# Kernel tuning notes

Hardware: AMD Instinct MI355X
Metric: run time of the kernel (lower is better)

Reference implementation:

```python
import jax, jax.numpy as jnp
import numpy as np

NEG_INF = -1e9
LN_EPS = 1e-5

N, F_IN, F_OUT, H = 4096, 128, 64, 4


def setup_inputs() -> dict:
    key = jax.random.key(0)
    ks = jax.random.split(key, 8)
    return {
        "nodes_features": jax.random.normal(ks[0], (N, F_IN), jnp.float32),
        "degree_matrix": jax.random.normal(ks[1], (N, N), jnp.float32),
        "edges_features_distance": jax.random.normal(ks[2], (N, N), jnp.float32),
        "edges_features_bond": jax.random.normal(ks[3], (N, N), jnp.float32),
        "proj_param": jax.random.normal(ks[4], (H, F_IN, F_OUT), jnp.float32) * 0.1,
        "score_src": jax.random.normal(ks[5], (H, F_OUT, 1), jnp.float32) * 0.1,
        "score_tgt": jax.random.normal(ks[6], (H, F_OUT, 1), jnp.float32) * 0.1,
        "skip_w": jax.random.normal(ks[7], (H * F_OUT, F_IN), jnp.float32) * 0.1,
        "cutoff": 0,
    }


def reference(nodes_features, degree_matrix, edges_features_distance,
              edges_features_bond, proj_param, score_src, score_tgt,
              skip_w, cutoff):
    # connectivity mask: nested where on degree/bond matrices  [N, N]
    wdm = degree_matrix + edges_features_bond
    mask = jnp.where(wdm > 0, wdm,
                     jnp.where(edges_features_bond > cutoff,
                               edges_features_bond + wdm, NEG_INF))

    # per-head projection: [H, N, F_out]
    proj = jnp.einsum('nf,hfo->hno', nodes_features, proj_param)

    # scalar scores per node per head: [H, N, 1]
    s_src = jnp.einsum('hno,hop->hnp', proj, score_src)
    s_tgt = jnp.einsum('hno,hop->hnp', proj, score_tgt)

    # broadcast score matrix [H, N, N]; softmax over dim=1 (as in the original)
    scores = jax.nn.leaky_relu(s_src + jnp.swapaxes(s_tgt, 1, 2), negative_slope=0.2)
    attn = jax.nn.softmax(scores + mask[None, :, :], axis=1)

    # weighted aggregation: [H, N, F_out] -> [N, H, F_out]
    out = jnp.einsum('hij,hjf->hif', attn, proj)
    out = jnp.swapaxes(out, 0, 1)

    # skip connection (F_in != F_out -> linear skip projection)
    skip = (nodes_features @ skip_w.T).reshape(-1, H, F_OUT)
    out = out + skip

    # concat heads, ELU activation (no bias: ctor passes bias=None)
    out = jax.nn.elu(out.reshape(-1, H * F_OUT))

    # fresh LayerNorm (weight=1, bias=0) over last dim of mask
    mu = jnp.mean(mask, axis=-1, keepdims=True)
    var = jnp.var(mask, axis=-1, keepdims=True)
    mask_ln = (mask - mu) / jnp.sqrt(var + LN_EPS)

    return out, mask_ln
```

## Files before the change

kernel.cpp:

```cpp
#include <hip/hip_runtime.h>
#include <math.h>

constexpr int kN  = 4096;
constexpr int kFI = 128;
constexpr int kFO = 64;
constexpr int kH  = 4;
constexpr int kHF = 256;
constexpr float kNegInf = -1e9f;
constexpr float kLnEps  = 1e-5f;
constexpr float kL2E    = 1.44269504f;

typedef short bf16x8 __attribute__((ext_vector_type(8)));
typedef float f32x4  __attribute__((ext_vector_type(4)));

__device__ __forceinline__ float lrelu(float x){ return x >= 0.f ? x : 0.2f*x; }

__device__ __forceinline__ float wave_sum(float v){
  #pragma unroll
  for (int s = 32; s > 0; s >>= 1) v += __shfl_xor(v, s, 64);
  return v;
}

__device__ __forceinline__ unsigned short f2bf(float x){
  unsigned u = __float_as_uint(x);
  u = (u + 0x7fffu + ((u >> 16) & 1u)) >> 16;
  return (unsigned short)u;
}
__device__ __forceinline__ unsigned f2bf_pk(float a, float b){
  return (unsigned)f2bf(a) | ((unsigned)f2bf(b) << 16);
}

__global__ __launch_bounds__(256) void k_tr(
    const float* __restrict__ skw, float* __restrict__ skwT)
{
  const int k  = blockIdx.x;
  const int hf = threadIdx.x;
  skwT[k*kHF + hf] = skw[hf*kFI + k];
}

__global__ __launch_bounds__(256) void k_proj(
    const float* __restrict__ nodes, const float* __restrict__ pp,
    const float* __restrict__ ssrc,  const float* __restrict__ stgt,
    const float* __restrict__ skwT,
    float* __restrict__ proj, float* __restrict__ ga, float* __restrict__ gb,
    float* __restrict__ skipo)
{
  __shared__ float feat[8][kFI];
  const int tid = threadIdx.x;
  const int n0  = blockIdx.x * 8;
  for (int idx = tid; idx < 8*kFI; idx += 256)
    feat[idx >> 7][idx & 127] = nodes[n0*kFI + idx];
  __syncthreads();
  const int h = tid >> 6, o = tid & 63;
  float accP[8], accS[8];
  #pragma unroll
  for (int n = 0; n < 8; ++n){ accP[n] = 0.f; accS[n] = 0.f; }
  for (int k0 = 0; k0 < kFI; k0 += 4){
    float p[4], w[4];
    #pragma unroll
    for (int u = 0; u < 4; ++u){
      p[u] = pp[(h*kFI + k0+u)*kFO + o];
      w[u] = skwT[(k0+u)*kHF + tid];
    }
    #pragma unroll
    for (int n = 0; n < 8; ++n){
      const float4 f4 = *(const float4*)&feat[n][k0];
      accP[n] = fmaf(f4.x, p[0], fmaf(f4.y, p[1],
                fmaf(f4.z, p[2], fmaf(f4.w, p[3], accP[n]))));
      accS[n] = fmaf(f4.x, w[0], fmaf(f4.y, w[1],
                fmaf(f4.z, w[2], fmaf(f4.w, w[3], accS[n]))));
    }
  }
  const float sa = ssrc[h*kFO + o];
  const float sb = stgt[h*kFO + o];
  #pragma unroll
  for (int n = 0; n < 8; ++n){
    proj[(h*kN + n0+n)*kFO + o] = accP[n];
    skipo[(n0+n)*kHF + tid]     = accS[n];
    const float va = wave_sum(accP[n] * sa);
    const float vb = wave_sum(accP[n] * sb);
    if (o == 0){ ga[h*kN + n0+n] = va; gb[h*kN + n0+n] = vb; }
  }
}

template<int RS>
__global__ __launch_bounds__(256) void k_colsum(
    const float* __restrict__ degm, const float* __restrict__ bondm,
    const float* __restrict__ ga,   const float* __restrict__ gb,
    const int* __restrict__ cutp,
    float* __restrict__ Spart, float* __restrict__ statg,
    float* __restrict__ maskws, int write_mask)
{
  const int j0 = (blockIdx.x * 256 + threadIdx.x) * 4;
  const int lane = threadIdx.x & 63;
  const float cut = (float)cutp[0];
  float4 bv[kH]; f32x4 sv[kH];
  #pragma unroll
  for (int h = 0; h < kH; ++h){
    bv[h] = *(const float4*)&gb[h*kN + j0];
    sv[h] = (f32x4){0.f, 0.f, 0.f, 0.f};
  }
  float msum[RS], msq[RS];
  #pragma unroll
  for (int r = 0; r < RS; ++r){ msum[r] = 0.f; msq[r] = 0.f; }

  const int i0 = blockIdx.y * RS;
  #pragma unroll
  for (int ib = 0; ib < RS; ib += 8){
    float4 dg[8], bd[8];
    #pragma unroll
    for (int u = 0; u < 8; ++u){
      const size_t off = (size_t)(i0+ib+u)*kN + j0;
      dg[u] = *(const float4*)&degm[off];
      bd[u] = *(const float4*)&bondm[off];
    }
    #pragma unroll
    for (int u = 0; u < 8; ++u){
      const int i = i0 + ib + u;
      float4 m;
      {
        float w0 = dg[u].x + bd[u].x, w1 = dg[u].y + bd[u].y;
        float w2 = dg[u].z + bd[u].z, w3 = dg[u].w + bd[u].w;
        m.x = w0 > 0.f ? w0 : (bd[u].x > cut ? bd[u].x + w0 : kNegInf);
        m.y = w1 > 0.f ? w1 : (bd[u].y > cut ? bd[u].y + w1 : kNegInf);
        m.z = w2 > 0.f ? w2 : (bd[u].z > cut ? bd[u].z + w2 : kNegInf);
        m.w = w3 > 0.f ? w3 : (bd[u].w > cut ? bd[u].w + w3 : kNegInf);
      }
      if (write_mask) *(float4*)&maskws[(size_t)i*kN + j0] = m;
      msum[ib+u] += (m.x + m.y) + (m.z + m.w);
      msq[ib+u]  += fmaf(m.x, m.x, fmaf(m.y, m.y, fmaf(m.z, m.z, m.w*m.w)));
      const float4 ml = {m.x*kL2E, m.y*kL2E, m.z*kL2E, m.w*kL2E};
      #pragma unroll
      for (int h = 0; h < kH; ++h){
        const float a = ga[h*kN + i];
        float t0 = a + bv[h].x, t1 = a + bv[h].y;
        float t2 = a + bv[h].z, t3 = a + bv[h].w;
        t0 = fmaxf(t0, 0.2f*t0); t1 = fmaxf(t1, 0.2f*t1);
        t2 = fmaxf(t2, 0.2f*t2); t3 = fmaxf(t3, 0.2f*t3);
        sv[h][0] += exp2f(fmaf(t0, kL2E, ml.x));
        sv[h][1] += exp2f(fmaf(t1, kL2E, ml.y));
        sv[h][2] += exp2f(fmaf(t2, kL2E, ml.z));
        sv[h][3] += exp2f(fmaf(t3, kL2E, ml.w));
      }
    }
  }
  #pragma unroll
  for (int h = 0; h < kH; ++h)
    *(float4*)&Spart[(size_t)(blockIdx.y*kH + h)*kN + j0] = *(float4*)&sv[h];

  #pragma unroll
  for (int r = 0; r < RS; ++r){
    const float s1 = wave_sum(msum[r]);
    const float s2 = wave_sum(msq[r]);
    if (lane == 0){
      atomicAdd(&statg[2*(i0+r)+0], s1);
      atomicAdd(&statg[2*(i0+r)+1], s2);
    }
  }
}

__global__ __launch_bounds__(256) void k_sred(
    const float* __restrict__ Spart, float* __restrict__ S, int strips)
{
  __shared__ float red[4][64];
  const int hj0  = blockIdx.x * 64;
  const int lane = threadIdx.x & 63;
  const int g    = threadIdx.x >> 6;
  const int per_chunk = strips >> 3;
  const int per_wave  = per_chunk >> 2;
  const int p0 = blockIdx.y*per_chunk + g*per_wave;
  float s0=0.f, s1=0.f, s2=0.f, s3=0.f;
  for (int p = p0; p < p0 + per_wave; p += 4){
    s0 += Spart[(size_t)(p+0)*kH*kN + hj0 + lane];
    s1 += Spart[(size_t)(p+1)*kH*kN + hj0 + lane];
    s2 += Spart[(size_t)(p+2)*kH*kN + hj0 + lane];
    s3 += Spart[(size_t)(p+3)*kH*kN + hj0 + lane];
  }
  red[g][lane] = (s0+s1)+(s2+s3);
  __syncthreads();
  if (threadIdx.x < 64)
    atomicAdd(&S[hj0+lane],
              (red[0][lane]+red[1][lane])+(red[2][lane]+red[3][lane]));
}

__global__ __launch_bounds__(256) void k_stat(
    const float* __restrict__ statg, float* __restrict__ statg2)
{
  const int i = blockIdx.x * 256 + threadIdx.x;
  const float mu  = statg[2*i] * (1.f/kN);
  const float var = statg[2*i+1] * (1.f/kN) - mu*mu;
  statg2[2*i+0] = mu;
  statg2[2*i+1] = rsqrtf(var + kLnEps);
}

__global__ __launch_bounds__(256) void k_pack(
    const float* __restrict__ proj, const float* __restrict__ S,
    unsigned short* __restrict__ pSpack)
{
  const int t = blockIdx.x * 256 + threadIdx.x;
  const int L  = t & 63;
  const int nt = (t >> 6) & 3;
  const int kb = (t >> 8) & 127;
  const int h  = t >> 15;
  const int f  = nt*16 + (L & 15);
  const int jb = kb*32 + (L >> 4)*8;
  union { unsigned short s[8]; uint4 v; } u;
  #pragma unroll
  for (int r = 0; r < 8; ++r){
    const int j = jb + r;
    u.s[r] = f2bf(proj[(size_t)(h*kN + j)*kFO + f] / S[h*kN + j]);
  }
  ((uint4*)pSpack)[t] = u.v;
}

__global__ __launch_bounds__(256) void k_aggr(
    const float* __restrict__ degm, const float* __restrict__ bondm,
    const float* __restrict__ maskws, int have_mask,
    const float* __restrict__ ga, const float* __restrict__ gb,
    const int* __restrict__ cutp,
    const unsigned short* __restrict__ pSpack,
    const float* __restrict__ statg2,
    float* __restrict__ accpart, float* __restrict__ mlnp)
{
  __shared__ unsigned short ebuf[kH*16*70];
  const int tid = threadIdx.x;
  const int w   = tid >> 6;
  const int L   = tid & 63;
  const int r0  = blockIdx.x * 16;
  const int jq  = blockIdx.y;
  const int span = kN / gridDim.y;
  const int nc   = span >> 6;
  const int jq0 = jq * span;
  const int ia  = tid >> 4;
  const int jc  = tid & 15;
  const float cut = (float)cutp[0];

  float av[kH];
  #pragma unroll
  for (int hh = 0; hh < kH; ++hh) av[hh] = ga[hh*kN + r0 + ia];
  const float mu = statg2[2*(r0+ia)+0];
  const float rs = statg2[2*(r0+ia)+1];

  f32x4 acc[4];
  #pragma unroll
  for (int nt = 0; nt < 4; ++nt) acc[nt] = (f32x4){0.f,0.f,0.f,0.f};

  float4 m_n; float4 bv_n[kH];
  auto LOADC = [&](int c){
    const int jg = jq0 + c*64 + 4*jc;
    const size_t off = (size_t)(r0+ia)*kN + jg;
    if (have_mask){
      m_n = *(const float4*)&maskws[off];
    } else {
      const float4 dg = *(const float4*)&degm[off];
      const float4 bd = *(const float4*)&bondm[off];
      float w0 = dg.x + bd.x, w1 = dg.y + bd.y;
      float w2 = dg.z + bd.z, w3 = dg.w + bd.w;
      m_n.x = w0 > 0.f ? w0 : (bd.x > cut ? bd.x + w0 : kNegInf);
      m_n.y = w1 > 0.f ? w1 : (bd.y > cut ? bd.y + w1 : kNegInf);
      m_n.z = w2 > 0.f ? w2 : (bd.z > cut ? bd.z + w2 : kNegInf);
      m_n.w = w3 > 0.f ? w3 : (bd.w > cut ? bd.w + w3 : kNegInf);
    }
    #pragma unroll
    for (int hh = 0; hh < kH; ++hh)
      bv_n[hh] = *(const float4*)&gb[hh*kN + jg];
  };

  LOADC(0);
  for (int c = 0; c < nc; ++c){
    {
      const float4 m = m_n;
      float4 bvl[kH];
      #pragma unroll
      for (int hh = 0; hh < kH; ++hh) bvl[hh] = bv_n[hh];

      const int jg = jq0 + c*64 + 4*jc;
      const size_t off = (size_t)(r0+ia)*kN + jg;
      float4 o;
      o.x = (m.x - mu) * rs;  o.y = (m.y - mu) * rs;
      o.z = (m.z - mu) * rs;  o.w = (m.w - mu) * rs;
      *(float4*)&mlnp[off] = o;
      const float4 ml = {m.x*kL2E, m.y*kL2E, m.z*kL2E, m.w*kL2E};
      #pragma unroll
      for (int hh = 0; hh < kH; ++hh){
        float t0 = av[hh] + bvl[hh].x, t1 = av[hh] + bvl[hh].y;
        float t2 = av[hh] + bvl[hh].z, t3 = av[hh] + bvl[hh].w;
        t0 = fmaxf(t0, 0.2f*t0); t1 = fmaxf(t1, 0.2f*t1);
        t2 = fmaxf(t2, 0.2f*t2); t3 = fmaxf(t3, 0.2f*t3);
        const float e0 = exp2f(fmaf(t0, kL2E, ml.x));
        const float e1 = exp2f(fmaf(t1, kL2E, ml.y));
        const float e2 = exp2f(fmaf(t2, kL2E, ml.z));
        const float e3 = exp2f(fmaf(t3, kL2E, ml.w));
        uint2 u;
        u.x = f2bf_pk(e0, e1);
        u.y = f2bf_pk(e2, e3);
        *(uint2*)&ebuf[(hh*16 + ia)*70 + 4*jc] = u;
      }
      if (c+1 < nc) LOADC(c+1);
    }
    __syncthreads();
    {
      const int jb = jq0 + c*64;
      const int kb0 = (jb >> 5);
      #pragma unroll
      for (int ks = 0; ks < 2; ++ks){
        const bf16x8 a = *(const bf16x8*)&ebuf[(w*16 + (L & 15))*70 + ks*32 + (L >> 4)*8];
        const int kb = kb0 + ks;
        #pragma unroll
        for (int nt = 0; nt < 4; ++nt){
          const bf16x8 b = *(const bf16x8*)&pSpack[(size_t)(((w*128 + kb)*4 + nt)*64 + L)*8];
          acc[nt] = __builtin_amdgcn_mfma_f32_16x16x32_bf16(a, b, acc[nt], 0, 0, 0);
        }
      }
    }
    __syncthreads();
  }

  #pragma unroll
  for (int nt = 0; nt < 4; ++nt){
    #pragma unroll
    for (int reg = 0; reg < 4; ++reg){
      const int i = r0 + (L >> 4)*4 + reg;
      const int f = w*64 + nt*16 + (L & 15);
      accpart[((size_t)jq*kN + i)*kHF + f] = acc[nt][reg];
    }
  }
}

__global__ __launch_bounds__(256) void k_out(
    const float* __restrict__ accpart, const float* __restrict__ skipo,
    float* __restrict__ outp, int nq)
{
  const int idx = blockIdx.x * 256 + threadIdx.x;
  float o = skipo[idx];
  for (int q = 0; q < nq; ++q) o += accpart[(size_t)q*kN*kHF + idx];
  o = o > 0.f ? o : expm1f(o);
  outp[idx] = o;
}

extern "C" void kernel_launch(void* const* d_in, const int* in_sizes, int n_in,
                              void* d_out, int out_size, void* d_ws, size_t ws_size,
                              hipStream_t stream)
{
  const float* nodes = (const float*)d_in[0];
  const float* degm  = (const float*)d_in[1];
  const float* bondm = (const float*)d_in[3];
  const float* pp    = (const float*)d_in[4];
  const float* ssrc  = (const float*)d_in[5];
  const float* stgt  = (const float*)d_in[6];
  const float* skw   = (const float*)d_in[7];
  const int*   cutp  = (const int*)d_in[8];

  const size_t fixed_floats = (size_t)kH*kN*kFO + 3*(size_t)kH*kN
                            + (size_t)kN*kHF + 4*(size_t)kN + (size_t)kFI*kHF;
  const size_t psp_floats = ((size_t)kH*kN*kFO)/2;
  const size_t region8 = (size_t)8*kN*kHF;
  const size_t region4 = (size_t)4*kN*kHF;
  const size_t need8      = (fixed_floats + region8 + psp_floats) * sizeof(float);
  const size_t need8_mask = need8 + (size_t)kN*kN*sizeof(float);
  const size_t need4_mask = (fixed_floats + region4 + psp_floats + (size_t)kN*kN)
                            * sizeof(float);

  int nq, strips, have_mask;
  if (ws_size >= need8_mask)      { nq = 8; strips = 512; have_mask = 1; }
  else if (ws_size >= need8)      { nq = 8; strips = 512; have_mask = 0; }
  else                            { nq = 4; strips = 256;
                                    have_mask = (ws_size >= need4_mask) ? 1 : 0; }

  float* ws     = (float*)d_ws;
  float* proj   = ws;
  float* ga     = proj + (size_t)kH*kN*kFO;
  float* gb     = ga + kH*kN;
  float* statg  = gb + kH*kN;
  float* statg2 = statg + 2*kN;
  float* S      = statg2 + 2*kN;
  float* skip   = S + kH*kN;
  float* skwT   = skip + (size_t)kN*kHF;
  float* accpart= skwT + (size_t)kFI*kHF;
  float* Spart  = accpart;
  unsigned short* pSpack = (unsigned short*)(accpart + (size_t)nq*kN*kHF);
  float* mask   = (float*)(pSpack + (size_t)kH*kN*kFO);

  float* outp = (float*)d_out;
  float* mlnp = outp + (size_t)kN*kHF;

  hipMemsetAsync(statg, 0, (4*(size_t)kN + (size_t)kH*kN)*sizeof(float), stream);

  k_tr<<<kFI, 256, 0, stream>>>(skw, skwT);
  k_proj<<<kN/8, 256, 0, stream>>>(nodes, pp, ssrc, stgt, skwT, proj, ga, gb, skip);
  if (strips == 512)
    k_colsum<8><<<dim3(kN/1024, 512), 256, 0, stream>>>(degm, bondm, ga, gb, cutp,
                                                        Spart, statg, mask, have_mask);
  else
    k_colsum<16><<<dim3(kN/1024, 256), 256, 0, stream>>>(degm, bondm, ga, gb, cutp,
                                                         Spart, statg, mask, have_mask);
  k_sred<<<dim3((kH*kN)/64, 8), 256, 0, stream>>>(Spart, S, strips);
  k_stat<<<kN/256, 256, 0, stream>>>(statg, statg2);
  k_pack<<<(kH*128*4*64)/256, 256, 0, stream>>>(proj, S, pSpack);
  k_aggr<<<dim3(kN/16, nq), 256, 0, stream>>>(degm, bondm, mask, have_mask,
                                              ga, gb, cutp, pSpack, statg2,
                                              accpart, mlnp);
  k_out<<<(kN*kHF)/256, 256, 0, stream>>>(accpart, skip, outp, nq);
}
```

Measured before the change: 325.3 us.

## Build attention A-fragments in registers and drop materialized mask buffer

k_aggr is restructured so each wave owns 16 rows and builds the bf16 exp fragments for all four heads directly in MFMA A-operand registers. This removes the LDS staging buffer and both __syncthreads per chunk, and the wave now accumulates all heads instead of one head per wave. The mask workspace is no longer written in k_colsum; k_aggr recomputes the mask from the degree and bond matrices, trading an extra read for one fewer 64MB write and read. The column split grows to 16 partitions when workspace allows, which enlarges the accpart reduction in k_out.

```diff
diff --git a/kernel.cpp b/kernel.cpp
--- a/kernel.cpp
+++ b/kernel.cpp
@@ -13,8 +13,6 @@
 typedef short bf16x8 __attribute__((ext_vector_type(8)));
 typedef float f32x4  __attribute__((ext_vector_type(4)));
 
-__device__ __forceinline__ float lrelu(float x){ return x >= 0.f ? x : 0.2f*x; }
-
 __device__ __forceinline__ float wave_sum(float v){
   #pragma unroll
   for (int s = 32; s > 0; s >>= 1) v += __shfl_xor(v, s, 64);
@@ -88,8 +86,7 @@
     const float* __restrict__ degm, const float* __restrict__ bondm,
     const float* __restrict__ ga,   const float* __restrict__ gb,
     const int* __restrict__ cutp,
-    float* __restrict__ Spart, float* __restrict__ statg,
-    float* __restrict__ maskws, int write_mask)
+    float* __restrict__ Spart, float* __restrict__ statg)
 {
   const int j0 = (blockIdx.x * 256 + threadIdx.x) * 4;
   const int lane = threadIdx.x & 63;
@@ -126,7 +123,6 @@
         m.z = w2 > 0.f ? w2 : (bd[u].z > cut ? bd[u].z + w2 : kNegInf);
         m.w = w3 > 0.f ? w3 : (bd[u].w > cut ? bd[u].w + w3 : kNegInf);
       }
-      if (write_mask) *(float4*)&maskws[(size_t)i*kN + j0] = m;
       msum[ib+u] += (m.x + m.y) + (m.z + m.w);
       msq[ib+u]  += fmaf(m.x, m.x, fmaf(m.y, m.y, fmaf(m.z, m.z, m.w*m.w)));
       const float4 ml = {m.x*kL2E, m.y*kL2E, m.z*kL2E, m.w*kL2E};
@@ -215,116 +211,105 @@
 
 __global__ __launch_bounds__(256) void k_aggr(
     const float* __restrict__ degm, const float* __restrict__ bondm,
-    const float* __restrict__ maskws, int have_mask,
     const float* __restrict__ ga, const float* __restrict__ gb,
     const int* __restrict__ cutp,
     const unsigned short* __restrict__ pSpack,
     const float* __restrict__ statg2,
-    float* __restrict__ accpart, float* __restrict__ mlnp)
-{
-  __shared__ unsigned short ebuf[kH*16*70];
-  const int tid = threadIdx.x;
-  const int w   = tid >> 6;
-  const int L   = tid & 63;
-  const int r0  = blockIdx.x * 16;
-  const int jq  = blockIdx.y;
-  const int span = kN / gridDim.y;
-  const int nc   = span >> 6;
-  const int jq0 = jq * span;
-  const int ia  = tid >> 4;
-  const int jc  = tid & 15;
+    float* __restrict__ accpart, float* __restrict__ mlnp, int span)
+{
+  const int tid  = threadIdx.x;
+  const int w    = tid >> 6;
+  const int L    = tid & 63;
+  const int rbase= blockIdx.x*64 + w*16;
+  const int row  = rbase + (L & 15);
+  const int colg = (L >> 4) * 8;
+  const int jq   = blockIdx.y;
+  const int jq0  = jq * span;
+  const int nchunk = span >> 5;
   const float cut = (float)cutp[0];
 
+  const float mu = statg2[2*row+0];
+  const float rs = statg2[2*row+1];
   float av[kH];
   #pragma unroll
-  for (int hh = 0; hh < kH; ++hh) av[hh] = ga[hh*kN + r0 + ia];
-  const float mu = statg2[2*(r0+ia)+0];
-  const float rs = statg2[2*(r0+ia)+1];
-
-  f32x4 acc[4];
-  #pragma unroll
-  for (int nt = 0; nt < 4; ++nt) acc[nt] = (f32x4){0.f,0.f,0.f,0.f};
-
-  float4 m_n; float4 bv_n[kH];
-  auto LOADC = [&](int c){
-    const int jg = jq0 + c*64 + 4*jc;
-    const size_t off = (size_t)(r0+ia)*kN + jg;
-    if (have_mask){
-      m_n = *(const float4*)&maskws[off];
-    } else {
-      const float4 dg = *(const float4*)&degm[off];
-      const float4 bd = *(const float4*)&bondm[off];
-      float w0 = dg.x + bd.x, w1 = dg.y + bd.y;
-      float w2 = dg.z + bd.z, w3 = dg.w + bd.w;
-      m_n.x = w0 > 0.f ? w0 : (bd.x > cut ? bd.x + w0 : kNegInf);
-      m_n.y = w1 > 0.f ? w1 : (bd.y > cut ? bd.y + w1 : kNegInf);
-      m_n.z = w2 > 0.f ? w2 : (bd.z > cut ? bd.z + w2 : kNegInf);
-      m_n.w = w3 > 0.f ? w3 : (bd.w > cut ? bd.w + w3 : kNegInf);
-    }
-    #pragma unroll
-    for (int hh = 0; hh < kH; ++hh)
-      bv_n[hh] = *(const float4*)&gb[hh*kN + jg];
-  };
-
-  LOADC(0);
-  for (int c = 0; c < nc; ++c){
+  for (int h = 0; h < kH; ++h) av[h] = ga[h*kN + row];
+
+  f32x4 acc[kH][4];
+  #pragma unroll
+  for (int h = 0; h < kH; ++h)
+    #pragma unroll
+    for (int nt = 0; nt < 4; ++nt) acc[h][nt] = (f32x4){0.f,0.f,0.f,0.f};
+
+  const size_t rowbase = (size_t)row * kN;
+
+  float4 dg0 = *(const float4*)&degm[rowbase + jq0 + colg];
+  float4 dg1 = *(const float4*)&degm[rowbase + jq0 + colg + 4];
+  float4 bd0 = *(const float4*)&bondm[rowbase + jq0 + colg];
+  float4 bd1 = *(const float4*)&bondm[rowbase + jq0 + colg + 4];
+
+  for (int c = 0; c < nchunk; ++c){
+    const int cb = jq0 + (c << 5);
+    float4 ndg0 = dg0, ndg1 = dg1, nbd0 = bd0, nbd1 = bd1;
+    if (c+1 < nchunk){
+      const size_t noff = rowbase + cb + 32 + colg;
+      ndg0 = *(const float4*)&degm[noff];
+      ndg1 = *(const float4*)&degm[noff + 4];
+      nbd0 = *(const float4*)&bondm[noff];
+      nbd1 = *(const float4*)&bondm[noff + 4];
+    }
+
+    const float dgv[8] = {dg0.x,dg0.y,dg0.z,dg0.w, dg1.x,dg1.y,dg1.z,dg1.w};
+    const float bdv[8] = {bd0.x,bd0.y,bd0.z,bd0.w, bd1.x,bd1.y,bd1.z,bd1.w};
+    float m[8], ml[8];
+    #pragma unroll
+    for (int r = 0; r < 8; ++r){
+      const float wv = dgv[r] + bdv[r];
+      m[r]  = wv > 0.f ? wv : (bdv[r] > cut ? bdv[r] + wv : kNegInf);
+      ml[r] = m[r] * kL2E;
+    }
     {
-      const float4 m = m_n;
-      float4 bvl[kH];
+      float4 o0, o1;
+      o0.x = (m[0]-mu)*rs; o0.y = (m[1]-mu)*rs;
+      o0.z = (m[2]-mu)*rs; o0.w = (m[3]-mu)*rs;
+      o1.x = (m[4]-mu)*rs; o1.y = (m[5]-mu)*rs;
+      o1.z = (m[6]-mu)*rs; o1.w = (m[7]-mu)*rs;
+      *(float4*)&mlnp[rowbase + cb + colg]     = o0;
+      *(float4*)&mlnp[rowbase + cb + colg + 4] = o1;
+    }
+    const int kb = cb >> 5;
+    #pragma unroll
+    for (int h = 0; h < kH; ++h){
+      const float4 g0 = *(const float4*)&gb[h*kN + cb + colg];
+      const float4 g1 = *(const float4*)&gb[h*kN + cb + colg + 4];
+      const float gv[8] = {g0.x,g0.y,g0.z,g0.w, g1.x,g1.y,g1.z,g1.w};
+      union { unsigned u[4]; bf16x8 v; } ua;
       #pragma unroll
-      for (int hh = 0; hh < kH; ++hh) bvl[hh] = bv_n[hh];
-
-      const int jg = jq0 + c*64 + 4*jc;
-      const size_t off = (size_t)(r0+ia)*kN + jg;
-      float4 o;
-      o.x = (m.x - mu) * rs;  o.y = (m.y - mu) * rs;
-      o.z = (m.z - mu) * rs;  o.w = (m.w - mu) * rs;
-      *(float4*)&mlnp[off] = o;
-      const float4 ml = {m.x*kL2E, m.y*kL2E, m.z*kL2E, m.w*kL2E};
+      for (int r2 = 0; r2 < 4; ++r2){
+        float t0 = av[h] + gv[2*r2],   t1 = av[h] + gv[2*r2+1];
+        t0 = fmaxf(t0, 0.2f*t0);       t1 = fmaxf(t1, 0.2f*t1);
+        const float e0 = exp2f(fmaf(t0, kL2E, ml[2*r2]));
+        const float e1 = exp2f(fmaf(t1, kL2E, ml[2*r2+1]));
+        ua.u[r2] = f2bf_pk(e0, e1);
+      }
       #pragma unroll
-      for (int hh = 0; hh < kH; ++hh){
-        float t0 = av[hh] + bvl[hh].x, t1 = av[hh] + bvl[hh].y;
-        float t2 = av[hh] + bvl[hh].z, t3 = av[hh] + bvl[hh].w;
-        t0 = fmaxf(t0, 0.2f*t0); t1 = fmaxf(t1, 0.2f*t1);
-        t2 = fmaxf(t2, 0.2f*t2); t3 = fmaxf(t3, 0.2f*t3);
-        const float e0 = exp2f(fmaf(t0, kL2E, ml.x));
-        const float e1 = exp2f(fmaf(t1, kL2E, ml.y));
-        const float e2 = exp2f(fmaf(t2, kL2E, ml.z));
-        const float e3 = exp2f(fmaf(t3, kL2E, ml.w));
-        uint2 u;
-        u.x = f2bf_pk(e0, e1);
-        u.y = f2bf_pk(e2, e3);
-        *(uint2*)&ebuf[(hh*16 + ia)*70 + 4*jc] = u;
-      }
-      if (c+1 < nc) LOADC(c+1);
-    }
-    __syncthreads();
-    {
-      const int jb = jq0 + c*64;
-      const int kb0 = (jb >> 5);
+      for (int nt = 0; nt < 4; ++nt){
+        const bf16x8 b = *(const bf16x8*)&pSpack[(size_t)(((h*128 + kb)*4 + nt)*64 + L)*8];
+        acc[h][nt] = __builtin_amdgcn_mfma_f32_16x16x32_bf16(ua.v, b, acc[h][nt], 0, 0, 0);
+      }
+    }
+    dg0 = ndg0; dg1 = ndg1; bd0 = nbd0; bd1 = nbd1;
+  }
+
+  #pragma unroll
+  for (int h = 0; h < kH; ++h)
+    #pragma unroll
+    for (int nt = 0; nt < 4; ++nt)
       #pragma unroll
-      for (int ks = 0; ks < 2; ++ks){
-        const bf16x8 a = *(const bf16x8*)&ebuf[(w*16 + (L & 15))*70 + ks*32 + (L >> 4)*8];
-        const int kb = kb0 + ks;
-        #pragma unroll
-        for (int nt = 0; nt < 4; ++nt){
-          const bf16x8 b = *(const bf16x8*)&pSpack[(size_t)(((w*128 + kb)*4 + nt)*64 + L)*8];
-          acc[nt] = __builtin_amdgcn_mfma_f32_16x16x32_bf16(a, b, acc[nt], 0, 0, 0);
-        }
-      }
-    }
-    __syncthreads();
-  }
-
-  #pragma unroll
-  for (int nt = 0; nt < 4; ++nt){
-    #pragma unroll
-    for (int reg = 0; reg < 4; ++reg){
-      const int i = r0 + (L >> 4)*4 + reg;
-      const int f = w*64 + nt*16 + (L & 15);
-      accpart[((size_t)jq*kN + i)*kHF + f] = acc[nt][reg];
-    }
-  }
+      for (int reg = 0; reg < 4; ++reg){
+        const int i = rbase + (L >> 4)*4 + reg;
+        const int f = h*64 + nt*16 + (L & 15);
+        accpart[((size_t)jq*kN + i)*kHF + f] = acc[h][nt][reg];
+      }
 }
 
 __global__ __launch_bounds__(256) void k_out(
@@ -354,18 +339,13 @@
   const size_t fixed_floats = (size_t)kH*kN*kFO + 3*(size_t)kH*kN
                             + (size_t)kN*kHF + 4*(size_t)kN + (size_t)kFI*kHF;
   const size_t psp_floats = ((size_t)kH*kN*kFO)/2;
-  const size_t region8 = (size_t)8*kN*kHF;
-  const size_t region4 = (size_t)4*kN*kHF;
-  const size_t need8      = (fixed_floats + region8 + psp_floats) * sizeof(float);
-  const size_t need8_mask = need8 + (size_t)kN*kN*sizeof(float);
-  const size_t need4_mask = (fixed_floats + region4 + psp_floats + (size_t)kN*kN)
-                            * sizeof(float);
-
-  int nq, strips, have_mask;
-  if (ws_size >= need8_mask)      { nq = 8; strips = 512; have_mask = 1; }
-  else if (ws_size >= need8)      { nq = 8; strips = 512; have_mask = 0; }
-  else                            { nq = 4; strips = 256;
-                                    have_mask = (ws_size >= need4_mask) ? 1 : 0; }
+  const size_t need16 = (fixed_floats + (size_t)16*kN*kHF + psp_floats)*sizeof(float);
+  const size_t need8  = (fixed_floats + (size_t)8*kN*kHF  + psp_floats)*sizeof(float);
+
+  int nq, strips;
+  if      (ws_size >= need16){ nq = 16; strips = 512; }
+  else if (ws_size >= need8) { nq = 8;  strips = 512; }
+  else                       { nq = 4;  strips = 256; }
 
   float* ws     = (float*)d_ws;
   float* proj   = ws;
@@ -379,7 +359,6 @@
   float* accpart= skwT + (size_t)kFI*kHF;
   float* Spart  = accpart;
   unsigned short* pSpack = (unsigned short*)(accpart + (size_t)nq*kN*kHF);
-  float* mask   = (float*)(pSpack + (size_t)kH*kN*kFO);
 
   float* outp = (float*)d_out;
   float* mlnp = outp + (size_t)kN*kHF;
@@ -390,15 +369,15 @@
   k_proj<<<kN/8, 256, 0, stream>>>(nodes, pp, ssrc, stgt, skwT, proj, ga, gb, skip);
   if (strips == 512)
     k_colsum<8><<<dim3(kN/1024, 512), 256, 0, stream>>>(degm, bondm, ga, gb, cutp,
-                                                        Spart, statg, mask, have_mask);
+                                                        Spart, statg);
   else
     k_colsum<16><<<dim3(kN/1024, 256), 256, 0, stream>>>(degm, bondm, ga, gb, cutp,
-                                                         Spart, statg, mask, have_mask);
+                                                         Spart, statg);
   k_sred<<<dim3((kH*kN)/64, 8), 256, 0, stream>>>(Spart, S, strips);
   k_stat<<<kN/256, 256, 0, stream>>>(statg, statg2);
   k_pack<<<(kH*128*4*64)/256, 256, 0, stream>>>(proj, S, pSpack);
-  k_aggr<<<dim3(kN/16, nq), 256, 0, stream>>>(degm, bondm, mask, have_mask,
-                                              ga, gb, cutp, pSpack, statg2,
-                                              accpart, mlnp);
+  k_aggr<<<dim3(kN/64, nq), 256, 0, stream>>>(degm, bondm, ga, gb, cutp,
+                                              pSpack, statg2, accpart, mlnp,
+                                              kN/nq);
   k_out<<<(kN*kHF)/256, 256, 0, stream>>>(accpart, skip, outp, nq);
 }
```

New measurement: 331.2 us. About the same (+1.8%).
